# Optimization experiments

Hardware: AMD Instinct MI355X
Metric: run time of the kernel (lower is better)

## Reference

```python
import jax, jax.numpy as jnp
import numpy as np

FULL_SCALE = 128
TOPK = 3
R = 0.5


def setup_inputs() -> dict:
    key = jax.random.key(0)
    k1, k2, k3, k4 = jax.random.split(key, 4)
    B, Na, Nb, D = 8, 4096, 4096, 64
    a_coords = jax.random.randint(k1, (B, Na, 3), 0, FULL_SCALE * 16, dtype=jnp.int32)
    b_coords = jax.random.randint(k2, (B, Nb, 3), 0, FULL_SCALE * 16, dtype=jnp.int32)
    a_feats = jax.random.normal(k3, (B, Na, D), dtype=jnp.float32)
    b_feats = jax.random.normal(k4, (B, Nb, D), dtype=jnp.float32)
    return {"a_feats": a_feats, "b_feats": b_feats,
            "a_coords": a_coords, "b_coords": b_coords}


def reference(a_feats, b_feats, a_coords, b_coords):
    # coords are divided by 16 (integer floor div) before the distance computation
    ca = (a_coords // 16).astype(jnp.float32)  # [B, Na, 3]
    cb = (b_coords // 16).astype(jnp.float32)  # [B, Nb, 3]

    # pairwise euclidean distance per batch group (torch.cdist equivalent)
    d2 = (jnp.sum(ca * ca, -1, keepdims=True)
          + jnp.sum(cb * cb, -1)[:, None, :]
          - 2.0 * jnp.einsum('bnd,bmd->bnm', ca, cb))  # [B, Na, Nb]
    dist = jnp.sqrt(jnp.clip(d2, 0.0, None)) / FULL_SCALE

    # top-k nearest neighbors (argsort ascending, take first TOPK)
    neg_top, idx = jax.lax.top_k(-dist, TOPK)  # idx: [B, Na, K]
    dist_w = R - jnp.clip(-neg_top, 0.0, R)    # [B, Na, K]

    # gather neighbor features: [B, Na, K, D]
    B = b_feats.shape[0]
    gathered = b_feats[jnp.arange(B)[:, None, None], idx]
    tmp = jnp.einsum('bnkd,bnk->bnd', gathered, dist_w)  # weighted sum over K

    # ME.cat(a, tmp): concatenate features along channel dim
    return jnp.concatenate([a_feats, tmp], axis=-1)  # [B, Na, 2D]
```

## Files before the change

### kernel.cpp

```cpp
#include <hip/hip_runtime.h>


#define NA 4096
#define NB 4096
#define FD 64
#define WPB 8
#define MPW 4
#define BLOCK (WPB * 64)
#define APB (WPB * MPW)

static __device__ __forceinline__ int med3_i32(int a, int b, int c) {
    int d;
    asm("v_med3_i32 %0, %1, %2, %3" : "=v"(d) : "v"(a), "v"(b), "v"(c));
    return d;
}

static __device__ __forceinline__ int mad_i24(int a, int b, int c) {
    int d;
    asm("v_mad_i32_i24 %0, %1, %2, %3" : "=v"(d) : "v"(a), "v"(b), "v"(c));
    return d;
}

__global__ __launch_bounds__(BLOCK, 8) void knn_gather_kernel(
    const float* __restrict__ a_feats,
    const float* __restrict__ b_feats,
    const int*   __restrict__ a_coords,
    const int*   __restrict__ b_coords,
    float* __restrict__ out)
{
    __shared__ int2 s_pg[NB];

    const int batch = blockIdx.y;
    const int tid   = threadIdx.x;

    const int* bc = b_coords + (size_t)batch * NB * 3;
    for (int i = tid; i < NB; i += BLOCK) {
        const int x = bc[3 * i + 0] >> 4;
        const int y = bc[3 * i + 1] >> 4;
        const int z = bc[3 * i + 2] >> 4;
        int2 v;
        v.x = x | (y << 8) | (z << 16);
        v.y = ((__mul24(x, x) + __mul24(y, y) + __mul24(z, z)) << 12) | i;
        s_pg[i] = v;
    }
    __syncthreads();

    const int wave  = tid >> 6;
    const int lane  = tid & 63;
    const int nbase = blockIdx.x * APB + wave * MPW;

    const int* ac = a_coords + ((size_t)batch * NA + nbase) * 3;
    int mx0, my0, mz0, mx1, my1, mz1, mx2, my2, mz2, mx3, my3, mz3;
    int aa0, aa1, aa2, aa3;
    {
        const int x0 = ac[0] >> 4, y0 = ac[1]  >> 4, z0 = ac[2]  >> 4;
        const int x1 = ac[3] >> 4, y1 = ac[4]  >> 4, z1 = ac[5]  >> 4;
        const int x2 = ac[6] >> 4, y2 = ac[7]  >> 4, z2 = ac[8]  >> 4;
        const int x3 = ac[9] >> 4, y3 = ac[10] >> 4, z3 = ac[11] >> 4;
        mx0 = -(x0 << 13); my0 = -(y0 << 13); mz0 = -(z0 << 13);
        mx1 = -(x1 << 13); my1 = -(y1 << 13); mz1 = -(z1 << 13);
        mx2 = -(x2 << 13); my2 = -(y2 << 13); mz2 = -(z2 << 13);
        mx3 = -(x3 << 13); my3 = -(y3 << 13); mz3 = -(z3 << 13);
        aa0 = __mul24(x0, x0) + __mul24(y0, y0) + __mul24(z0, z0);
        aa1 = __mul24(x1, x1) + __mul24(y1, y1) + __mul24(z1, z1);
        aa2 = __mul24(x2, x2) + __mul24(y2, y2) + __mul24(z2, z2);
        aa3 = __mul24(x3, x3) + __mul24(y3, y3) + __mul24(z3, z3);
    }

    int k0_0 = 0x7FFFFFFF, k1_0 = 0x7FFFFFFF, k2_0 = 0x7FFFFFFF;
    int k0_1 = 0x7FFFFFFF, k1_1 = 0x7FFFFFFF, k2_1 = 0x7FFFFFFF;
    int k0_2 = 0x7FFFFFFF, k1_2 = 0x7FFFFFFF, k2_2 = 0x7FFFFFFF;
    int k0_3 = 0x7FFFFFFF, k1_3 = 0x7FFFFFFF, k2_3 = 0x7FFFFFFF;

    const int4* pg4 = (const int4*)s_pg;

#define KNN_PG(PP, GG)                                               \
    {                                                                \
        const int P  = (PP);                                         \
        const int G  = (GG);                                         \
        const int bx = P & 0xFF;                                     \
        const int by = (P >> 8) & 0xFF;                              \
        const int bz = P >> 16;                                      \
        {   const int u = mad_i24(bz, mz0,                           \
                          mad_i24(by, my0, mad_i24(bx, mx0, G)));    \
            const int n0 = min(k0_0, u);                             \
            const int n1 = med3_i32(k0_0, k1_0, u);                  \
            const int n2 = med3_i32(k1_0, k2_0, u);                  \
            k0_0 = n0; k1_0 = n1; k2_0 = n2; }                       \
        {   const int u = mad_i24(bz, mz1,                           \
                          mad_i24(by, my1, mad_i24(bx, mx1, G)));    \
            const int n0 = min(k0_1, u);                             \
            const int n1 = med3_i32(k0_1, k1_1, u);                  \
            const int n2 = med3_i32(k1_1, k2_1, u);                  \
            k0_1 = n0; k1_1 = n1; k2_1 = n2; }                       \
        {   const int u = mad_i24(bz, mz2,                           \
                          mad_i24(by, my2, mad_i24(bx, mx2, G)));    \
            const int n0 = min(k0_2, u);                             \
            const int n1 = med3_i32(k0_2, k1_2, u);                  \
            const int n2 = med3_i32(k1_2, k2_2, u);                  \
            k0_2 = n0; k1_2 = n1; k2_2 = n2; }                       \
        {   const int u = mad_i24(bz, mz3,                           \
                          mad_i24(by, my3, mad_i24(bx, mx3, G)));    \
            const int n0 = min(k0_3, u);                             \
            const int n1 = med3_i32(k0_3, k1_3, u);                  \
            const int n2 = med3_i32(k1_3, k2_3, u);                  \
            k0_3 = n0; k1_3 = n1; k2_3 = n2; }                       \
    }

#pragma unroll 2
    for (int k = 0; k < 16; ++k) {
        const int base = k << 7;
        const int4 X = pg4[base + lane];
        const int4 Y = pg4[base + 64 + lane];
        KNN_PG(X.x, X.y)
        KNN_PG(X.z, X.w)
        KNN_PG(Y.x, Y.y)
        KNN_PG(Y.z, Y.w)
    }
#undef KNN_PG

    const float* bfb = b_feats + (size_t)batch * NB * FD;
    int K0[MPW] = {k0_0, k0_1, k0_2, k0_3};
    int K1[MPW] = {k1_0, k1_1, k1_2, k1_3};
    int K2[MPW] = {k2_0, k2_1, k2_2, k2_3};
    const int AA[MPW] = {aa0, aa1, aa2, aa3};

#pragma unroll
    for (int m = 0; m < MPW; ++m) {
        int a0 = K0[m], a1 = K1[m], a2 = K2[m];
#pragma unroll
        for (int d = 1; d < 64; d <<= 1) {
            const int b0 = __shfl_xor(a0, d, 64);
            const int b1 = __shfl_xor(a1, d, 64);
            const int b2 = __shfl_xor(a2, d, 64);
            const int h0 = max(a0, b0);
            const int l1 = min(a1, b1);
            const int c2 = min(a2, b2);
            a0 = min(a0, b0);
            a1 = min(h0, l1);
            a2 = med3_i32(c2, l1, h0);
        }
        const int i0 = a0 & 4095, i1 = a1 & 4095, i2 = a2 & 4095;
        const float d0 = sqrtf((float)((a0 >> 12) + AA[m])) * (1.0f / 128.0f);
        const float d1 = sqrtf((float)((a1 >> 12) + AA[m])) * (1.0f / 128.0f);
        const float d2 = sqrtf((float)((a2 >> 12) + AA[m])) * (1.0f / 128.0f);
        const float w0 = 0.5f - fminf(d0, 0.5f);
        const float w1 = 0.5f - fminf(d1, 0.5f);
        const float w2 = 0.5f - fminf(d2, 0.5f);

        const size_t row = (size_t)batch * NA + (nbase + m);
        const float g = w0 * bfb[i0 * FD + lane]
                      + w1 * bfb[i1 * FD + lane]
                      + w2 * bfb[i2 * FD + lane];
        out[row * 128 + lane]      = a_feats[row * FD + lane];
        out[row * 128 + 64 + lane] = g;
    }
}

extern "C" void kernel_launch(void* const* d_in, const int* in_sizes, int n_in,
                              void* d_out, int out_size, void* d_ws, size_t ws_size,
                              hipStream_t stream) {
    const float* a_feats  = (const float*)d_in[0];
    const float* b_feats  = (const float*)d_in[1];
    const int*   a_coords = (const int*)d_in[2];
    const int*   b_coords = (const int*)d_in[3];
    float* out = (float*)d_out;

    const int B = in_sizes[0] / (NA * FD);
    dim3 grid(NA / APB, B);
    knn_gather_kernel<<<grid, BLOCK, 0, stream>>>(a_feats, b_feats, a_coords,
                                                  b_coords, out);
}
```

Measured before the change: 105.7 us.

## Replace brute-force KNN with uniform-grid cell search and expanding shells

```diff
diff --git a/kernel.cpp b/kernel.cpp
--- a/kernel.cpp
+++ b/kernel.cpp
@@ -1,38 +1,190 @@
 #include <hip/hip_runtime.h>
+#include <limits.h>
 
 
 #define NA 4096
 #define NB 4096
 #define FD 64
+
+static __device__ __forceinline__ int med3_i32(int a, int b, int c) {
+    int d;
+    asm("v_med3_i32 %0, %1, %2, %3" : "=v"(d) : "v"(a), "v"(b), "v"(c));
+    return d;
+}
+
+static __device__ __forceinline__ int mad_i24(int a, int b, int c) {
+    int d;
+    asm("v_mad_i32_i24 %0, %1, %2, %3" : "=v"(d) : "v"(a), "v"(b), "v"(c));
+    return d;
+}
+
+__global__ __launch_bounds__(256) void build_cells(
+    const int* __restrict__ b_coords,
+    int2* __restrict__ table,
+    int*  __restrict__ starts)
+{
+    __shared__ int hist[4096];
+    __shared__ int wsum[4];
+    const int batch = blockIdx.x;
+    const int tid   = threadIdx.x;
+    const int lane  = tid & 63, wave = tid >> 6;
+
+    for (int i = tid; i < 4096; i += 256) hist[i] = 0;
+    __syncthreads();
+
+    const int* bc = b_coords + (size_t)batch * NB * 3;
+    int cellv[16], pk[16];
+#pragma unroll
+    for (int j = 0; j < 16; ++j) {
+        const int i = tid + j * 256;
+        const int x = bc[3 * i + 0] >> 4;
+        const int y = bc[3 * i + 1] >> 4;
+        const int z = bc[3 * i + 2] >> 4;
+        pk[j]    = x | (y << 8) | (z << 16);
+        cellv[j] = ((z >> 3) << 8) | ((y >> 3) << 4) | (x >> 3);
+        atomicAdd(&hist[cellv[j]], 1);
+    }
+    __syncthreads();
+
+    const int base = tid << 4;
+    int loc[16];
+    int sum = 0;
+#pragma unroll
+    for (int j = 0; j < 16; ++j) { loc[j] = sum; sum += hist[base + j]; }
+    int inc = sum;
+    for (int d = 1; d < 64; d <<= 1) {
+        const int u = __shfl_up(inc, d, 64);
+        if (lane >= d) inc += u;
+    }
+    if (lane == 63) wsum[wave] = inc;
+    __syncthreads();
+    int woff = 0;
+    for (int w = 0; w < 4; ++w) if (w < wave) woff += wsum[w];
+    const int excl = woff + inc - sum;
+
+    int* st = starts + (size_t)batch * 4096;
+#pragma unroll
+    for (int j = 0; j < 16; ++j) {
+        const int s = excl + loc[j];
+        hist[base + j] = s;
+        st[base + j]   = s;
+    }
+    __syncthreads();
+
+    int2* tb = table + (size_t)batch * NB;
+#pragma unroll
+    for (int j = 0; j < 16; ++j) {
+        const int slot = atomicAdd(&hist[cellv[j]], 1);
+        int2 e; e.x = pk[j]; e.y = tid + j * 256;
+        tb[slot] = e;
+    }
+}
+
+__global__ __launch_bounds__(128) void query_gather(
+    const float* __restrict__ a_feats,
+    const float* __restrict__ b_feats,
+    const int*   __restrict__ a_coords,
+    const int2*  __restrict__ table,
+    const int*   __restrict__ starts,
+    float* __restrict__ out)
+{
+    __shared__ int2 s_tab[4096];
+    __shared__ unsigned short s_start[4096];
+    __shared__ int s_keys[128 * 3];
+
+    const int tid   = threadIdx.x;
+    const int batch = blockIdx.x >> 5;
+    const int qbase = (blockIdx.x & 31) * 128;
+
+    const int2* tb = table  + (size_t)batch * NB;
+    const int*  st = starts + (size_t)batch * 4096;
+    for (int i = tid; i < 4096; i += 128) {
+        s_tab[i]   = tb[i];
+        s_start[i] = (unsigned short)st[i];
+    }
+    __syncthreads();
+
+    const int q  = qbase + tid;
+    const int* ac = a_coords + ((size_t)batch * NA + q) * 3;
+    const int ax = ac[0] >> 4, ay = ac[1] >> 4, az = ac[2] >> 4;
+    const int cx = ax >> 3, cy = ay >> 3, cz = az >> 3;
+
+    int k0 = INT_MAX, k1 = INT_MAX, k2 = INT_MAX;
+
+    for (int r = 0; r < 16; ++r) {
+        for (int dz = -r; dz <= r; ++dz) {
+            const int z = cz + dz;
+            if ((unsigned)z > 15u) continue;
+            const bool ez = (dz == -r) | (dz == r);
+            for (int dy = -r; dy <= r; ++dy) {
+                const int y = cy + dy;
+                if ((unsigned)y > 15u) continue;
+                const bool ey = (dy == -r) | (dy == r);
+                const int step = (ez | ey) ? 1 : (2 * r);
+                for (int dx = -r; dx <= r; dx += step) {
+                    const int x = cx + dx;
+                    if ((unsigned)x > 15u) continue;
+                    const int cell = (z << 8) | (y << 4) | x;
+                    const int jsb = s_start[cell];
+                    const int jeb = (cell == 4095) ? NB : (int)s_start[cell + 1];
+                    for (int j = jsb; j < jeb; ++j) {
+                        const int2 e = s_tab[j];
+                        const int bx = e.x & 255;
+                        const int by = (e.x >> 8) & 255;
+                        const int bz = e.x >> 16;
+                        const int du = ax - bx, dv = ay - by, dw = az - bz;
+                        const int d2 = mad_i24(du, du,
+                                       mad_i24(dv, dv, __mul24(dw, dw)));
+                        const int key = (d2 << 12) | e.y;
+                        const int n0 = min(k0, key);
+                        const int n1 = med3_i32(k0, k1, key);
+                        const int n2 = med3_i32(k1, k2, key);
+                        k0 = n0; k1 = n1; k2 = n2;
+                    }
+                }
+            }
+        }
+        const int rr = 8 * r + 1;
+        if (k2 < ((rr * rr) << 12)) break;
+    }
+
+    s_keys[tid * 3 + 0] = k0;
+    s_keys[tid * 3 + 1] = k1;
+    s_keys[tid * 3 + 2] = k2;
+    __syncthreads();
+
+    const int lane = tid & 63, wave = tid >> 6;
+    const float* bfb = b_feats + (size_t)batch * NB * FD;
+    for (int qq = wave; qq < 128; qq += 2) {
+        const int K0 = s_keys[qq * 3 + 0];
+        const int K1 = s_keys[qq * 3 + 1];
+        const int K2 = s_keys[qq * 3 + 2];
+        const int i0 = K0 & 4095, i1 = K1 & 4095, i2 = K2 & 4095;
+        const float w0 = 0.5f - fminf(sqrtf((float)(K0 >> 12)) * (1.0f / 128.0f), 0.5f);
+        const float w1 = 0.5f - fminf(sqrtf((float)(K1 >> 12)) * (1.0f / 128.0f), 0.5f);
+        const float w2 = 0.5f - fminf(sqrtf((float)(K2 >> 12)) * (1.0f / 128.0f), 0.5f);
+        const size_t row = (size_t)batch * NA + (qbase + qq);
+        const float g = w0 * bfb[i0 * FD + lane]
+                      + w1 * bfb[i1 * FD + lane]
+                      + w2 * bfb[i2 * FD + lane];
+        out[row * 128 + lane]      = a_feats[row * FD + lane];
+        out[row * 128 + 64 + lane] = g;
+    }
+}
+
 #define WPB 8
 #define MPW 4
 #define BLOCK (WPB * 64)
 #define APB (WPB * MPW)
 
-static __device__ __forceinline__ int med3_i32(int a, int b, int c) {
-    int d;
-    asm("v_med3_i32 %0, %1, %2, %3" : "=v"(d) : "v"(a), "v"(b), "v"(c));
-    return d;
-}
-
-static __device__ __forceinline__ int mad_i24(int a, int b, int c) {
-    int d;
-    asm("v_mad_i32_i24 %0, %1, %2, %3" : "=v"(d) : "v"(a), "v"(b), "v"(c));
-    return d;
-}
-
 __global__ __launch_bounds__(BLOCK, 8) void knn_gather_kernel(
-    const float* __restrict__ a_feats,
-    const float* __restrict__ b_feats,
-    const int*   __restrict__ a_coords,
-    const int*   __restrict__ b_coords,
+    const float* __restrict__ a_feats, const float* __restrict__ b_feats,
+    const int* __restrict__ a_coords, const int* __restrict__ b_coords,
     float* __restrict__ out)
 {
     __shared__ int2 s_pg[NB];
-
     const int batch = blockIdx.y;
     const int tid   = threadIdx.x;
-
     const int* bc = b_coords + (size_t)batch * NB * 3;
     for (int i = tid; i < NB; i += BLOCK) {
         const int x = bc[3 * i + 0] >> 4;
@@ -44,11 +196,9 @@
         s_pg[i] = v;
     }
     __syncthreads();
-
     const int wave  = tid >> 6;
     const int lane  = tid & 63;
     const int nbase = blockIdx.x * APB + wave * MPW;
-
     const int* ac = a_coords + ((size_t)batch * NA + nbase) * 3;
     int mx0, my0, mz0, mx1, my1, mz1, mx2, my2, mz2, mx3, my3, mz3;
     int aa0, aa1, aa2, aa3;
@@ -66,14 +216,11 @@
         aa2 = __mul24(x2, x2) + __mul24(y2, y2) + __mul24(z2, z2);
         aa3 = __mul24(x3, x3) + __mul24(y3, y3) + __mul24(z3, z3);
     }
-
     int k0_0 = 0x7FFFFFFF, k1_0 = 0x7FFFFFFF, k2_0 = 0x7FFFFFFF;
     int k0_1 = 0x7FFFFFFF, k1_1 = 0x7FFFFFFF, k2_1 = 0x7FFFFFFF;
     int k0_2 = 0x7FFFFFFF, k1_2 = 0x7FFFFFFF, k2_2 = 0x7FFFFFFF;
     int k0_3 = 0x7FFFFFFF, k1_3 = 0x7FFFFFFF, k2_3 = 0x7FFFFFFF;
-
     const int4* pg4 = (const int4*)s_pg;
-
 #define KNN_PG(PP, GG)                                               \
     {                                                                \
         const int P  = (PP);                                         \
@@ -106,7 +253,6 @@
             const int n2 = med3_i32(k1_3, k2_3, u);                  \
             k0_3 = n0; k1_3 = n1; k2_3 = n2; }                       \
     }
-
 #pragma unroll 2
     for (int k = 0; k < 16; ++k) {
         const int base = k << 7;
@@ -118,13 +264,11 @@
         KNN_PG(Y.z, Y.w)
     }
 #undef KNN_PG
-
     const float* bfb = b_feats + (size_t)batch * NB * FD;
     int K0[MPW] = {k0_0, k0_1, k0_2, k0_3};
     int K1[MPW] = {k1_0, k1_1, k1_2, k1_3};
     int K2[MPW] = {k2_0, k2_1, k2_2, k2_3};
     const int AA[MPW] = {aa0, aa1, aa2, aa3};
-
 #pragma unroll
     for (int m = 0; m < MPW; ++m) {
         int a0 = K0[m], a1 = K1[m], a2 = K2[m];
@@ -147,7 +291,6 @@
         const float w0 = 0.5f - fminf(d0, 0.5f);
         const float w1 = 0.5f - fminf(d1, 0.5f);
         const float w2 = 0.5f - fminf(d2, 0.5f);
-
         const size_t row = (size_t)batch * NA + (nbase + m);
         const float g = w0 * bfb[i0 * FD + lane]
                       + w1 * bfb[i1 * FD + lane]
@@ -167,7 +310,18 @@
     float* out = (float*)d_out;
 
     const int B = in_sizes[0] / (NA * FD);
-    dim3 grid(NA / APB, B);
-    knn_gather_kernel<<<grid, BLOCK, 0, stream>>>(a_feats, b_feats, a_coords,
-                                                  b_coords, out);
-}
+    const size_t need = (size_t)B * NB * sizeof(int2)
+                      + (size_t)B * 4096 * sizeof(int);
+
+    if (ws_size >= need) {
+        int2* table  = (int2*)d_ws;
+        int*  starts = (int*)((char*)d_ws + (size_t)B * NB * sizeof(int2));
+        build_cells<<<B, 256, 0, stream>>>(b_coords, table, starts);
+        query_gather<<<B * 32, 128, 0, stream>>>(a_feats, b_feats, a_coords,
+                                                 table, starts, out);
+    } else {
+        dim3 grid(NA / APB, B);
+        knn_gather_kernel<<<grid, BLOCK, 0, stream>>>(a_feats, b_feats,
+                                                      a_coords, b_coords, out);
+    }
+}
```

After: 147.2 us. 39.3% more time.
